# Performance work log

Hardware: AMD Instinct MI355X
Metric: run time of the kernel (lower is better)

The kernel has to match this reference:

```python
import jax, jax.numpy as jnp
import numpy as np

E = 2_000_000   # edges
N = 200_000     # atoms
B = 100         # bond types (10 species, ordered pairs)
R = 13          # reduced_matrix_element (SK integrals per bond)
G = 512         # num_xgrid
T = 10          # atom types
OE = 4          # n_onsite_Es
R_MIN, R_MAX = 1.0, 6.0  # SK table distance range (Bohr-ish)


def setup_inputs() -> dict:
    key = jax.random.key(0)
    k1, k2, k3, k4, k5, k6 = jax.random.split(key, 6)
    rij = jax.random.uniform(k1, (E,), jnp.float32, 1.5, 5.5)
    edge_type = jax.random.randint(k2, (E,), 0, B, jnp.int32)
    atom_type = jax.random.randint(k3, (N,), 0, T, jnp.int32)
    xx = jnp.linspace(R_MIN, R_MAX, G, dtype=jnp.float32)  # sorted distance grid
    hopping_param = jax.random.normal(k4, (B, R, G), jnp.float32)
    overlap_param = jax.random.normal(k5, (B, R, G), jnp.float32)
    onsite_param = jax.random.normal(k6, (T, OE, 1), jnp.float32)
    return {"rij": rij, "edge_type": edge_type, "atom_type": atom_type,
            "xx": xx, "hopping_param": hopping_param,
            "overlap_param": overlap_param, "onsite_param": onsite_param}


def _interp_by_type(rij, edge_type, xx, table):
    """Fused gather + linear interpolation, keyed by edge_type.

    Replaces the original per-bond-type masked loop: for each edge, pick the
    [R, G] SK table for its bond type and linearly interpolate along the
    distance grid at rij. Returns [E, R].
    """
    g = xx.shape[0]
    # interval index for each edge (clamped -> linear extrapolation at edges)
    idx = jnp.clip(jnp.searchsorted(xx, rij, side="right") - 1, 0, g - 2)  # [E]
    x0 = xx[idx]
    x1 = xx[idx + 1]
    t = ((rij - x0) / (x1 - x0))[:, None]  # [E, 1]
    # advanced indexing on axes 0 and 2, full slice on axis 1 -> [E, R]
    y0 = table[edge_type, :, idx]
    y1 = table[edge_type, :, idx + 1]
    return y0 * (1.0 - t) + y1 * t


def reference(rij, edge_type, atom_type, xx, hopping_param, overlap_param, onsite_param):
    edge_features = _interp_by_type(rij, edge_type, xx, hopping_param)   # [E, R]
    edge_overlap = _interp_by_type(rij, edge_type, xx, overlap_param)    # [E, R]
    # dftb onsite: direct per-atom-type parameter lookup (num_paras == 1)
    node_features = onsite_param[atom_type, :, 0]                         # [N, OE]
    return edge_features, edge_overlap, node_features
```

## Files before the change

kernel.cpp:

```cpp
#include <hip/hip_runtime.h>

#define E_CNT 2000000
#define N_CNT 200000
#define B_CNT 100
#define R_CNT 13
#define G_CNT 512
#define T_CNT 10
#define OE_CNT 4

#define P_ROW 16
#define P_ONE ((size_t)B_CNT * G_CNT * P_ROW)
#define P_BYTES_TOTAL (2 * P_ONE * 4)

#define EDGES_PER_BLOCK 64
#define EDGE_BLOCKS (E_CNT / EDGES_PER_BLOCK)
#define NODE_BLOCKS ((N_CNT + 255) / 256)
#define OUT_OVL_OFF ((size_t)E_CNT * R_CNT)
#define OUT_NODE_OFF ((size_t)2 * E_CNT * R_CNT)

#define SH_STRIDE 20

__global__ __launch_bounds__(256) void repack2_kernel(
    const float* __restrict__ hopping,
    const float* __restrict__ overlap,
    float* __restrict__ Ph,
    float* __restrict__ Po)
{
    int tid = blockIdx.x * 256 + threadIdx.x;
    int g = tid & (G_CNT - 1);
    int br = tid >> 9;
    int r = br % R_CNT;
    int b = br / R_CNT;
    size_t src = (size_t)tid;
    size_t dst = ((size_t)(b * G_CNT + g)) * P_ROW + r;
    Ph[dst] = hopping[src];
    Po[dst] = overlap[src];
}

template <bool DO_NODES>
__global__ __launch_bounds__(256) void pass_kernel(
    const float* __restrict__ rij,
    const int*   __restrict__ edge_type,
    const float* __restrict__ P,
    const int*   __restrict__ atom_type,
    const float* __restrict__ onsite,
    float* __restrict__ out,
    float* __restrict__ out_nodes)
{
    if (blockIdx.x < EDGE_BLOCKS) {
        __shared__ float sh[EDGES_PER_BLOCK * SH_STRIDE];

        int tid = threadIdx.x;
        int eL = tid >> 2;
        int j  = tid & 3;
        int e  = blockIdx.x * EDGES_PER_BLOCK + eL;

        float r = rij[e];
        int b = edge_type[e];

        const float inv_dx = 511.0f / 5.0f;
        float s = (r - 1.0f) * inv_dx;
        int idx = (int)s;
        idx = max(0, min(G_CNT - 2, idx));
        float t = s - (float)idx;
        float omt = 1.0f - t;

        size_t base = ((size_t)((b << 9) + idx)) * P_ROW + 4 * j;
        float4 y0 = *(const float4*)(P + base);
        float4 y1 = *(const float4*)(P + base + P_ROW);

        float4 v;
        v.x = y0.x * omt + y1.x * t;
        v.y = y0.y * omt + y1.y * t;
        v.z = y0.z * omt + y1.z * t;
        v.w = y0.w * omt + y1.w * t;

        *(float4*)(sh + eL * SH_STRIDE + 4 * j) = v;
        __syncthreads();

        if (tid < 208) {
            unsigned f0 = (unsigned)tid * 4u;
            float4 q;
            float* qs = (float*)&q;
            #pragma unroll
            for (int k = 0; k < 4; ++k) {
                unsigned f = f0 + k;
                unsigned ee = f / 13u;
                unsigned rr = f - ee * 13u;
                qs[k] = sh[ee * SH_STRIDE + rr];
            }
            *(float4*)(out + (size_t)blockIdx.x * (EDGES_PER_BLOCK * R_CNT) + f0) = q;
        }
    } else if (DO_NODES) {
        int n = (blockIdx.x - EDGE_BLOCKS) * 256 + threadIdx.x;
        if (n < N_CNT) {
            int t = atom_type[n];
            float4 v;
            v.x = onsite[t * OE_CNT + 0];
            v.y = onsite[t * OE_CNT + 1];
            v.z = onsite[t * OE_CNT + 2];
            v.w = onsite[t * OE_CNT + 3];
            *(float4*)(out_nodes + (size_t)n * OE_CNT) = v;
        }
    }
}

__global__ __launch_bounds__(256) void dftbsk_fallback(
    const float* __restrict__ rij,
    const int*   __restrict__ edge_type,
    const int*   __restrict__ atom_type,
    const float* __restrict__ xx,
    const float* __restrict__ hopping,
    const float* __restrict__ overlap,
    const float* __restrict__ onsite,
    float*       __restrict__ out)
{
    __shared__ float sxx[G_CNT];
    for (int i = threadIdx.x; i < G_CNT; i += blockDim.x) sxx[i] = xx[i];
    __syncthreads();

    long long gid = (long long)blockIdx.x * blockDim.x + threadIdx.x;
    if (gid < E_CNT) {
        int e = (int)gid;
        float r = rij[e];
        int b = edge_type[e];
        const float inv_dx = (float)(G_CNT - 1) / 5.0f;
        int idx = (int)floorf((r - 1.0f) * inv_dx);
        idx = max(0, min(G_CNT - 2, idx));
        while (idx > 0 && r < sxx[idx]) --idx;
        while (idx < G_CNT - 2 && r >= sxx[idx + 1]) ++idx;
        float x0 = sxx[idx], x1 = sxx[idx + 1];
        float t = (r - x0) / (x1 - x0);
        float omt = 1.0f - t;
        const float* hb = hopping + (size_t)b * (R_CNT * G_CNT) + idx;
        const float* ob = overlap + (size_t)b * (R_CNT * G_CNT) + idx;
        float* outh = out + (size_t)e * R_CNT;
        float* outo = out + OUT_OVL_OFF + (size_t)e * R_CNT;
        #pragma unroll
        for (int rr = 0; rr < R_CNT; ++rr)
            outh[rr] = hb[rr * G_CNT] * omt + hb[rr * G_CNT + 1] * t;
        #pragma unroll
        for (int rr = 0; rr < R_CNT; ++rr)
            outo[rr] = ob[rr * G_CNT] * omt + ob[rr * G_CNT + 1] * t;
    } else if (gid < (long long)E_CNT + N_CNT) {
        int n = (int)(gid - E_CNT);
        int t = atom_type[n];
        float4 v;
        v.x = onsite[t * OE_CNT + 0];
        v.y = onsite[t * OE_CNT + 1];
        v.z = onsite[t * OE_CNT + 2];
        v.w = onsite[t * OE_CNT + 3];
        *(float4*)(out + OUT_NODE_OFF + (size_t)n * OE_CNT) = v;
    }
}

extern "C" void kernel_launch(void* const* d_in, const int* in_sizes, int n_in,
                              void* d_out, int out_size, void* d_ws, size_t ws_size,
                              hipStream_t stream) {
    const float* rij        = (const float*)d_in[0];
    const int*   edge_type  = (const int*)d_in[1];
    const int*   atom_type  = (const int*)d_in[2];
    const float* xx         = (const float*)d_in[3];
    const float* hopping    = (const float*)d_in[4];
    const float* overlap    = (const float*)d_in[5];
    const float* onsite     = (const float*)d_in[6];
    float* out = (float*)d_out;

    if (ws_size >= P_BYTES_TOTAL) {
        float* Ph = (float*)d_ws;
        float* Po = Ph + P_ONE;
        const int repack_total = B_CNT * R_CNT * G_CNT;
        repack2_kernel<<<repack_total / 256, 256, 0, stream>>>(hopping, overlap, Ph, Po);
        pass_kernel<true><<<EDGE_BLOCKS + NODE_BLOCKS, 256, 0, stream>>>(
            rij, edge_type, Ph, atom_type, onsite, out, out + OUT_NODE_OFF);
        pass_kernel<false><<<EDGE_BLOCKS, 256, 0, stream>>>(
            rij, edge_type, Po, atom_type, onsite, out + OUT_OVL_OFF, out + OUT_NODE_OFF);
    } else {
        const long long total = (long long)E_CNT + N_CNT;
        const int grid = (int)((total + 255) / 256);
        dftbsk_fallback<<<grid, 256, 0, stream>>>(rij, edge_type, atom_type, xx,
                                                  hopping, overlap, onsite, out);
    }
}
```

Measured before the change: 279.5 us.

## Fuse hopping and overlap passes into one kernel with nontemporal streaming

```diff
diff --git a/kernel.cpp b/kernel.cpp
--- a/kernel.cpp
+++ b/kernel.cpp
@@ -7,6 +7,8 @@
 #define G_CNT 512
 #define T_CNT 10
 #define OE_CNT 4
+
+typedef float nfloat4 __attribute__((ext_vector_type(4)));
 
 #define P_ROW 16
 #define P_ONE ((size_t)B_CNT * G_CNT * P_ROW)
@@ -18,7 +20,7 @@
 #define OUT_OVL_OFF ((size_t)E_CNT * R_CNT)
 #define OUT_NODE_OFF ((size_t)2 * E_CNT * R_CNT)
 
-#define SH_STRIDE 20
+#define SH_STRIDE 32
 
 __global__ __launch_bounds__(256) void repack2_kernel(
     const float* __restrict__ hopping,
@@ -37,15 +39,14 @@
     Po[dst] = overlap[src];
 }
 
-template <bool DO_NODES>
-__global__ __launch_bounds__(256) void pass_kernel(
+__global__ __launch_bounds__(256) void dftbsk_fused(
     const float* __restrict__ rij,
     const int*   __restrict__ edge_type,
-    const float* __restrict__ P,
+    const float* __restrict__ Ph,
+    const float* __restrict__ Po,
     const int*   __restrict__ atom_type,
     const float* __restrict__ onsite,
-    float* __restrict__ out,
-    float* __restrict__ out_nodes)
+    float* __restrict__ out)
 {
     if (blockIdx.x < EDGE_BLOCKS) {
         __shared__ float sh[EDGES_PER_BLOCK * SH_STRIDE];
@@ -55,8 +56,8 @@
         int j  = tid & 3;
         int e  = blockIdx.x * EDGES_PER_BLOCK + eL;
 
-        float r = rij[e];
-        int b = edge_type[e];
+        float r = __builtin_nontemporal_load(rij + e);
+        int   b = __builtin_nontemporal_load(edge_type + e);
 
         const float inv_dx = 511.0f / 5.0f;
         float s = (r - 1.0f) * inv_dx;
@@ -66,41 +67,50 @@
         float omt = 1.0f - t;
 
         size_t base = ((size_t)((b << 9) + idx)) * P_ROW + 4 * j;
-        float4 y0 = *(const float4*)(P + base);
-        float4 y1 = *(const float4*)(P + base + P_ROW);
+        float4 h0 = *(const float4*)(Ph + base);
+        float4 h1 = *(const float4*)(Ph + base + P_ROW);
+        float4 o0 = *(const float4*)(Po + base);
+        float4 o1 = *(const float4*)(Po + base + P_ROW);
 
-        float4 v;
-        v.x = y0.x * omt + y1.x * t;
-        v.y = y0.y * omt + y1.y * t;
-        v.z = y0.z * omt + y1.z * t;
-        v.w = y0.w * omt + y1.w * t;
+        float4 v, w;
+        v.x = h0.x * omt + h1.x * t;  v.y = h0.y * omt + h1.y * t;
+        v.z = h0.z * omt + h1.z * t;  v.w = h0.w * omt + h1.w * t;
+        w.x = o0.x * omt + o1.x * t;  w.y = o0.y * omt + o1.y * t;
+        w.z = o0.z * omt + o1.z * t;  w.w = o0.w * omt + o1.w * t;
 
         *(float4*)(sh + eL * SH_STRIDE + 4 * j) = v;
+        *(float4*)(sh + eL * SH_STRIDE + 16 + 4 * j) = w;
         __syncthreads();
 
-        if (tid < 208) {
-            unsigned f0 = (unsigned)tid * 4u;
-            float4 q;
-            float* qs = (float*)&q;
-            #pragma unroll
-            for (int k = 0; k < 4; ++k) {
-                unsigned f = f0 + k;
-                unsigned ee = f / 13u;
-                unsigned rr = f - ee * 13u;
-                qs[k] = sh[ee * SH_STRIDE + rr];
+        size_t outBase = (size_t)blockIdx.x * (EDGES_PER_BLOCK * R_CNT);
+        #pragma unroll
+        for (int L = 0; L < 2; ++L) {
+            int i4 = tid + L * 256;
+            if (i4 < 416) {
+                bool isOvl = i4 >= 208;
+                unsigned f0 = (unsigned)(isOvl ? (i4 - 208) : i4) * 4u;
+                nfloat4 q;
+                #pragma unroll
+                for (int k = 0; k < 4; ++k) {
+                    unsigned f = f0 + k;
+                    unsigned ee = f / 13u;
+                    unsigned rr = f - ee * 13u;
+                    q[k] = sh[ee * SH_STRIDE + (isOvl ? 16 : 0) + rr];
+                }
+                float* dst = out + (isOvl ? OUT_OVL_OFF : 0) + outBase + f0;
+                __builtin_nontemporal_store(q, (nfloat4*)dst);
             }
-            *(float4*)(out + (size_t)blockIdx.x * (EDGES_PER_BLOCK * R_CNT) + f0) = q;
         }
-    } else if (DO_NODES) {
+    } else {
         int n = (blockIdx.x - EDGE_BLOCKS) * 256 + threadIdx.x;
         if (n < N_CNT) {
             int t = atom_type[n];
-            float4 v;
-            v.x = onsite[t * OE_CNT + 0];
-            v.y = onsite[t * OE_CNT + 1];
-            v.z = onsite[t * OE_CNT + 2];
-            v.w = onsite[t * OE_CNT + 3];
-            *(float4*)(out_nodes + (size_t)n * OE_CNT) = v;
+            nfloat4 v;
+            v[0] = onsite[t * OE_CNT + 0];
+            v[1] = onsite[t * OE_CNT + 1];
+            v[2] = onsite[t * OE_CNT + 2];
+            v[3] = onsite[t * OE_CNT + 3];
+            __builtin_nontemporal_store(v, (nfloat4*)(out + OUT_NODE_OFF + (size_t)n * OE_CNT));
         }
     }
 }
@@ -171,10 +181,8 @@
         float* Po = Ph + P_ONE;
         const int repack_total = B_CNT * R_CNT * G_CNT;
         repack2_kernel<<<repack_total / 256, 256, 0, stream>>>(hopping, overlap, Ph, Po);
-        pass_kernel<true><<<EDGE_BLOCKS + NODE_BLOCKS, 256, 0, stream>>>(
-            rij, edge_type, Ph, atom_type, onsite, out, out + OUT_NODE_OFF);
-        pass_kernel<false><<<EDGE_BLOCKS, 256, 0, stream>>>(
-            rij, edge_type, Po, atom_type, onsite, out + OUT_OVL_OFF, out + OUT_NODE_OFF);
+        dftbsk_fused<<<EDGE_BLOCKS + NODE_BLOCKS, 256, 0, stream>>>(
+            rij, edge_type, Ph, Po, atom_type, onsite, out);
     } else {
         const long long total = (long long)E_CNT + N_CNT;
         const int grid = (int)((total + 255) / 256);
```

Result: no change. 281.2 us (+0.6%).
